# Kernel optimization log

Measured on AMD Instinct MI355X. Metric: run time of the kernel, lower is better.

## Reference

```python
import jax, jax.numpy as jnp
import numpy as np

SIZE = 7
SIGMA = 1.5
K1 = 0.01
K2 = 0.03
DATA_RANGE = 2.0
NP_ = SIZE * SIZE
COV_NORM = NP_ / (NP_ - 1)
PAD = SIZE // 2


def _gaussian_window(size=SIZE, sigma=SIGMA, channels=1):
    x = np.arange(size) - size // 2
    g = np.exp(-x**2 / (2.0 * sigma**2))[None, :]
    g = (g.T @ g)
    g = g / g.sum()
    w = np.tile(g[None, None], (channels, 1, 1, 1))  # [C,1,size,size]
    return jnp.asarray(w, dtype=jnp.float32)


def _dwconv(x, w):
    # depthwise conv2d, zero padding PAD, stride 1; x: [N,C,H,W], w: [C,1,k,k]
    c = x.shape[1]
    return jax.lax.conv_general_dilated(
        x, w, window_strides=(1, 1), padding=[(PAD, PAD), (PAD, PAD)],
        dimension_numbers=('NCHW', 'OIHW', 'NCHW'), feature_group_count=c)


def setup_inputs() -> dict:
    key = jax.random.key(0)
    k1, k2 = jax.random.split(key)
    X = jax.random.uniform(k1, (64, 1, 320, 320), dtype=jnp.float32)
    Y = jax.random.uniform(k2, (64, 1, 320, 320), dtype=jnp.float32)
    window = _gaussian_window()
    return {"X": X, "Y": Y, "window": window}


def reference(X, Y, window):
    C1 = (K1 * DATA_RANGE) ** 2
    C2 = (K2 * DATA_RANGE) ** 2
    mux = _dwconv(X, window)
    muy = _dwconv(Y, window)
    mux_sq = mux * mux
    muy_sq = muy * muy
    muxy = mux * muy
    sigmax_sq = (_dwconv(X * X, window) - mux_sq) * COV_NORM
    sigmay_sq = (_dwconv(Y * Y, window) - muy_sq) * COV_NORM
    sigmaxy = (_dwconv(X * Y, window) - muxy) * COV_NORM
    ssim_map = ((2 * muxy + C1) * (2 * sigmaxy + C2)) / \
               ((mux_sq + muy_sq + C1) * (sigmax_sq + sigmay_sq + C2))
    return 1.0 - ssim_map.mean()
```

## Files before the change

### kernel.cpp

```cpp
#include <hip/hip_runtime.h>
#include <math.h>


#define WI 320
#define HI 320
#define NI 64
#define TWO 58
#define GXD 6
#define GYD 20
#define NBLK (GXD * GYD * NI)
#define NPIX ((double)NI * WI * HI)
#define WREG (5 * 4 * 64)

typedef float v4 __attribute__((ext_vector_type(4)));

struct W7 { float w[7]; };

template <bool YI, int XM>
__device__ __forceinline__ float wave_task(
    const float* __restrict__ Xn, const float* __restrict__ Yn,
    const W7& wv, float* __restrict__ vb, int x0, int y0, int lane)
{
    const int gx   = x0 + lane - 3;
    const bool xok = (XM == 1) || (XM == 0 ? (gx >= 0) : (gx < WI));

    float xr[10], yr[10];
#pragma unroll
    for (int j = 0; j < 10; ++j) {
        const int gy  = y0 + j - 3;
        const bool ok = xok && (YI || ((unsigned)gy < (unsigned)HI));
        float xv = 0.f, yv = 0.f;
        if (ok) { const int idx = gy * WI + gx; xv = Xn[idx]; yv = Yn[idx]; }
        xr[j] = xv; yr[j] = yv;
    }

    float acc[5][4];
#pragma unroll
    for (int ch = 0; ch < 5; ++ch)
#pragma unroll
        for (int r = 0; r < 4; ++r) acc[ch][r] = 0.f;
#pragma unroll
    for (int j = 0; j < 10; ++j) {
        const float xv = xr[j], yv = yr[j];
        const float pxx = xv * xv, pyy = yv * yv, pxy = xv * yv;
#pragma unroll
        for (int r = 0; r < 4; ++r) {
            const int d = j - r;
            if (d >= 0 && d < 7) {
                const float w = wv.w[d];
                acc[0][r] += w * xv;
                acc[1][r] += w * yv;
                acc[2][r] += w * pxx;
                acc[3][r] += w * pyy;
                acc[4][r] += w * pxy;
            }
        }
    }
#pragma unroll
    for (int ch = 0; ch < 5; ++ch)
#pragma unroll
        for (int r = 0; r < 4; ++r)
            vb[ch * 256 + r * 64 + lane] = acc[ch][r];

    __builtin_amdgcn_wave_barrier();

    float lsum = 0.f;
    const int row = lane >> 4;
    const int xg  = (lane & 15) << 2;
    if (xg < TWO) {
        const float C1 = 0.0004f, C2 = 0.0036f, COVN = 49.f / 48.f;
        float m[4][5];
#pragma unroll
        for (int j = 0; j < 4; ++j)
#pragma unroll
            for (int ch = 0; ch < 5; ++ch) m[j][ch] = 0.f;
#pragma unroll
        for (int ch = 0; ch < 5; ++ch) {
            const v4* p = (const v4*)&vb[ch * 256 + row * 64 + xg];
            v4 a = p[0], b = p[1], c = p[2];
            float f[12] = {a.x,a.y,a.z,a.w, b.x,b.y,b.z,b.w, c.x,c.y,c.z,c.w};
#pragma unroll
            for (int j = 0; j < 4; ++j) {
                float s = 0.f;
#pragma unroll
                for (int d = 0; d < 7; ++d) s += wv.w[d] * f[j + d];
                m[j][ch] = s;
            }
        }
#pragma unroll
        for (int j = 0; j < 4; ++j) {
            const float mx = m[j][0], my = m[j][1];
            const float mxsq = mx * mx;
            const float mysq = my * my;
            const float mxy  = mx * my;
            const float vx   = (m[j][2] - mxsq) * COVN;
            const float vy   = (m[j][3] - mysq) * COVN;
            const float vxy  = (m[j][4] - mxy)  * COVN;
            const float num  = (2.f * mxy + C1) * (2.f * vxy + C2);
            const float den  = (mxsq + mysq + C1) * (vx + vy + C2);
            const bool valid = (xg + j < TWO) && (XM != 2 || x0 + xg + j < WI);
            lsum += valid ? num * __builtin_amdgcn_rcpf(den) : 0.f;
        }
    }
    return lsum;
}

__global__ __launch_bounds__(256) void ssim_kernel(
    const float* __restrict__ X, const float* __restrict__ Y,
    W7 wv, float* __restrict__ partial)
{
    __shared__ __align__(16) float vbuf[4 * WREG + 16];
    __shared__ float wsum[4];

    const int tid  = threadIdx.x;
    const int lane = tid & 63;
    const int w    = tid >> 6;
    const int x0   = blockIdx.x * TWO;
    const int y0   = blockIdx.y * 16 + w * 4;
    const float* __restrict__ Xn = X + (size_t)blockIdx.z * (WI * HI);
    const float* __restrict__ Yn = Y + (size_t)blockIdx.z * (WI * HI);
    float* vb = vbuf + w * WREG;

    const bool yi = (y0 >= 3) && (y0 <= HI - 7);
    const int  xm = (blockIdx.x == 0) ? 0 : ((blockIdx.x == GXD - 1) ? 2 : 1);

    float lsum;
    if (yi) {
        if      (xm == 0) lsum = wave_task<true, 0>(Xn, Yn, wv, vb, x0, y0, lane);
        else if (xm == 1) lsum = wave_task<true, 1>(Xn, Yn, wv, vb, x0, y0, lane);
        else              lsum = wave_task<true, 2>(Xn, Yn, wv, vb, x0, y0, lane);
    } else {
        if      (xm == 0) lsum = wave_task<false, 0>(Xn, Yn, wv, vb, x0, y0, lane);
        else if (xm == 1) lsum = wave_task<false, 1>(Xn, Yn, wv, vb, x0, y0, lane);
        else              lsum = wave_task<false, 2>(Xn, Yn, wv, vb, x0, y0, lane);
    }

#pragma unroll
    for (int off = 32; off > 0; off >>= 1)
        lsum += __shfl_down(lsum, off, 64);
    if (lane == 0) wsum[w] = lsum;
    __syncthreads();
    if (tid == 0) {
        const int bid = (blockIdx.z * GYD + blockIdx.y) * GXD + blockIdx.x;
        partial[bid] = (wsum[0] + wsum[1]) + (wsum[2] + wsum[3]);
    }
}

__global__ __launch_bounds__(256) void ssim_finalize(
    const float* __restrict__ partial, float* __restrict__ out)
{
    __shared__ double ws[4];
    const int tid = threadIdx.x;
    double s = 0.0;
    for (int i = tid; i < NBLK; i += 256) s += (double)partial[i];
#pragma unroll
    for (int off = 32; off > 0; off >>= 1)
        s += __shfl_down(s, off, 64);
    if ((tid & 63) == 0) ws[tid >> 6] = s;
    __syncthreads();
    if (tid == 0)
        out[0] = (float)(1.0 - ((ws[0] + ws[1]) + (ws[2] + ws[3])) / NPIX);
}

extern "C" void kernel_launch(void* const* d_in, const int* in_sizes, int n_in,
                              void* d_out, int out_size, void* d_ws, size_t ws_size,
                              hipStream_t stream) {
    const float* X = (const float*)d_in[0];
    const float* Y = (const float*)d_in[1];
    W7 wv;
    {
        double g[7], s = 0.0;
        for (int i = 0; i < 7; ++i) {
            double x = (double)(i - 3);
            g[i] = exp(-(x * x) / (2.0 * 1.5 * 1.5));
            s += g[i];
        }
        for (int i = 0; i < 7; ++i) wv.w[i] = (float)(g[i] / s);
    }

    float* partial = (float*)d_ws;

    dim3 grid(GXD, GYD, NI);
    ssim_kernel<<<grid, 256, 0, stream>>>(X, Y, wv, partial);
    ssim_finalize<<<1, 256, 0, stream>>>(partial, (float*)d_out);
}
```

Baseline: 111.0 us.

## Process eight rows per wave in single-wave blocks to cut halo reloads

Each wave now computes an 8-row strip instead of 4, so the 6-row vertical halo is amortized over more output rows. Blocks shrink to one wave, which removes the cross-wave shared reduction and __syncthreads. The horizontal pass is remapped to 8 lanes per row with 8 outputs each, using a padded row stride of 68. The trade-offs are higher register pressure from the larger accumulator arrays and a block count that doubles relative to the old layout.

```diff
diff --git a/kernel.cpp b/kernel.cpp
--- a/kernel.cpp
+++ b/kernel.cpp
@@ -7,10 +7,13 @@
 #define NI 64
 #define TWO 58
 #define GXD 6
-#define GYD 20
+#define RPW 8
+#define GYD (HI / RPW)
 #define NBLK (GXD * GYD * NI)
 #define NPIX ((double)NI * WI * HI)
-#define WREG (5 * 4 * 64)
+#define RSTR 68
+#define CSTR (RPW * RSTR)
+#define WREG (5 * CSTR)
 
 typedef float v4 __attribute__((ext_vector_type(4)));
 
@@ -24,9 +27,9 @@
     const int gx   = x0 + lane - 3;
     const bool xok = (XM == 1) || (XM == 0 ? (gx >= 0) : (gx < WI));
 
-    float xr[10], yr[10];
+    float xr[RPW + 6], yr[RPW + 6];
 #pragma unroll
-    for (int j = 0; j < 10; ++j) {
+    for (int j = 0; j < RPW + 6; ++j) {
         const int gy  = y0 + j - 3;
         const bool ok = xok && (YI || ((unsigned)gy < (unsigned)HI));
         float xv = 0.f, yv = 0.f;
@@ -34,17 +37,17 @@
         xr[j] = xv; yr[j] = yv;
     }
 
-    float acc[5][4];
+    float acc[5][RPW];
 #pragma unroll
     for (int ch = 0; ch < 5; ++ch)
 #pragma unroll
-        for (int r = 0; r < 4; ++r) acc[ch][r] = 0.f;
+        for (int r = 0; r < RPW; ++r) acc[ch][r] = 0.f;
 #pragma unroll
-    for (int j = 0; j < 10; ++j) {
+    for (int j = 0; j < RPW + 6; ++j) {
         const float xv = xr[j], yv = yr[j];
         const float pxx = xv * xv, pyy = yv * yv, pxy = xv * yv;
 #pragma unroll
-        for (int r = 0; r < 4; ++r) {
+        for (int r = 0; r < RPW; ++r) {
             const int d = j - r;
             if (d >= 0 && d < 7) {
                 const float w = wv.w[d];
@@ -59,28 +62,29 @@
 #pragma unroll
     for (int ch = 0; ch < 5; ++ch)
 #pragma unroll
-        for (int r = 0; r < 4; ++r)
-            vb[ch * 256 + r * 64 + lane] = acc[ch][r];
+        for (int r = 0; r < RPW; ++r)
+            vb[ch * CSTR + r * RSTR + lane] = acc[ch][r];
 
     __builtin_amdgcn_wave_barrier();
 
     float lsum = 0.f;
-    const int row = lane >> 4;
-    const int xg  = (lane & 15) << 2;
-    if (xg < TWO) {
+    const int row = lane >> 3;
+    const int xg  = (lane & 7) << 3;
+    {
         const float C1 = 0.0004f, C2 = 0.0036f, COVN = 49.f / 48.f;
-        float m[4][5];
+        float m[RPW][5];
 #pragma unroll
-        for (int j = 0; j < 4; ++j)
+        for (int j = 0; j < RPW; ++j)
 #pragma unroll
             for (int ch = 0; ch < 5; ++ch) m[j][ch] = 0.f;
 #pragma unroll
         for (int ch = 0; ch < 5; ++ch) {
-            const v4* p = (const v4*)&vb[ch * 256 + row * 64 + xg];
-            v4 a = p[0], b = p[1], c = p[2];
-            float f[12] = {a.x,a.y,a.z,a.w, b.x,b.y,b.z,b.w, c.x,c.y,c.z,c.w};
+            const v4* p = (const v4*)&vb[ch * CSTR + row * RSTR + xg];
+            v4 a = p[0], b = p[1], c = p[2], d4 = p[3];
+            float f[16] = {a.x,a.y,a.z,a.w, b.x,b.y,b.z,b.w,
+                           c.x,c.y,c.z,c.w, d4.x,d4.y,d4.z,d4.w};
 #pragma unroll
-            for (int j = 0; j < 4; ++j) {
+            for (int j = 0; j < RPW; ++j) {
                 float s = 0.f;
 #pragma unroll
                 for (int d = 0; d < 7; ++d) s += wv.w[d] * f[j + d];
@@ -88,7 +92,7 @@
             }
         }
 #pragma unroll
-        for (int j = 0; j < 4; ++j) {
+        for (int j = 0; j < RPW; ++j) {
             const float mx = m[j][0], my = m[j][1];
             const float mxsq = mx * mx;
             const float mysq = my * my;
@@ -105,44 +109,38 @@
     return lsum;
 }
 
-__global__ __launch_bounds__(256) void ssim_kernel(
+__global__ __launch_bounds__(64) void ssim_kernel(
     const float* __restrict__ X, const float* __restrict__ Y,
     W7 wv, float* __restrict__ partial)
 {
-    __shared__ __align__(16) float vbuf[4 * WREG + 16];
-    __shared__ float wsum[4];
+    __shared__ __align__(16) float vbuf[WREG + 16];
 
-    const int tid  = threadIdx.x;
-    const int lane = tid & 63;
-    const int w    = tid >> 6;
+    const int lane = threadIdx.x;
     const int x0   = blockIdx.x * TWO;
-    const int y0   = blockIdx.y * 16 + w * 4;
+    const int y0   = blockIdx.y * RPW;
     const float* __restrict__ Xn = X + (size_t)blockIdx.z * (WI * HI);
     const float* __restrict__ Yn = Y + (size_t)blockIdx.z * (WI * HI);
-    float* vb = vbuf + w * WREG;
 
-    const bool yi = (y0 >= 3) && (y0 <= HI - 7);
+    const bool yi = (y0 >= 3) && (y0 <= HI - RPW - 3);
     const int  xm = (blockIdx.x == 0) ? 0 : ((blockIdx.x == GXD - 1) ? 2 : 1);
 
     float lsum;
     if (yi) {
-        if      (xm == 0) lsum = wave_task<true, 0>(Xn, Yn, wv, vb, x0, y0, lane);
-        else if (xm == 1) lsum = wave_task<true, 1>(Xn, Yn, wv, vb, x0, y0, lane);
-        else              lsum = wave_task<true, 2>(Xn, Yn, wv, vb, x0, y0, lane);
+        if      (xm == 0) lsum = wave_task<true, 0>(Xn, Yn, wv, vbuf, x0, y0, lane);
+        else if (xm == 1) lsum = wave_task<true, 1>(Xn, Yn, wv, vbuf, x0, y0, lane);
+        else              lsum = wave_task<true, 2>(Xn, Yn, wv, vbuf, x0, y0, lane);
     } else {
-        if      (xm == 0) lsum = wave_task<false, 0>(Xn, Yn, wv, vb, x0, y0, lane);
-        else if (xm == 1) lsum = wave_task<false, 1>(Xn, Yn, wv, vb, x0, y0, lane);
-        else              lsum = wave_task<false, 2>(Xn, Yn, wv, vb, x0, y0, lane);
+        if      (xm == 0) lsum = wave_task<false, 0>(Xn, Yn, wv, vbuf, x0, y0, lane);
+        else if (xm == 1) lsum = wave_task<false, 1>(Xn, Yn, wv, vbuf, x0, y0, lane);
+        else              lsum = wave_task<false, 2>(Xn, Yn, wv, vbuf, x0, y0, lane);
     }
 
 #pragma unroll
     for (int off = 32; off > 0; off >>= 1)
         lsum += __shfl_down(lsum, off, 64);
-    if (lane == 0) wsum[w] = lsum;
-    __syncthreads();
-    if (tid == 0) {
+    if (lane == 0) {
         const int bid = (blockIdx.z * GYD + blockIdx.y) * GXD + blockIdx.x;
-        partial[bid] = (wsum[0] + wsum[1]) + (wsum[2] + wsum[3]);
+        partial[bid] = lsum;
     }
 }
 
@@ -181,6 +179,6 @@
     float* partial = (float*)d_ws;
 
     dim3 grid(GXD, GYD, NI);
-    ssim_kernel<<<grid, 256, 0, stream>>>(X, Y, wv, partial);
+    ssim_kernel<<<grid, 64, 0, stream>>>(X, Y, wv, partial);
     ssim_finalize<<<1, 256, 0, stream>>>(partial, (float*)d_out);
 }
```

Result: slower. 117.5 us (+5.8%).
